# Kernel tuning notes

Measured on AMD Instinct MI355X. Metric: run time of the kernel, lower is better.

The kernel has to match this reference:

```python
import jax, jax.numpy as jnp
import numpy as np
import math


def _forward(x, f0, theta, sigma, theta0, fbs, mix, w1, b1, w2, b2, conv_w):
    B, I, H, W = x.shape          # config requires B == I == H (== W here)
    S, O, _ = f0.shape            # config requires O == 1
    # ---- log-Gabor filter bank, fully vectorized over (scale, out, in) ----
    yy = jnp.linspace(-1.0, 1.0, H)[:, None]   # meshgrid 'ij': y along rows
    xx = jnp.linspace(-1.0, 1.0, W)[None, :]
    r = jnp.sqrt(xx ** 2 + yy ** 2 + 1e-6)     # [H,W]
    phi = jnp.arctan2(yy, xx)                  # [H,W]
    lr = jnp.log(r)
    log_gabor = jnp.exp(-(lr - jnp.log(f0)[..., None, None]) ** 2
                        / (2.0 * jnp.log(sigma)[..., None, None] ** 2))
    angular = jnp.exp(-(phi - theta[..., None, None]) ** 2
                      / (2.0 * theta0[..., None, None] ** 2))
    filters = log_gabor * angular              # [S,O,I,H,W]
    # ---- FFT (torch fftshift default shifts ALL dims; jnp matches) ----
    xs = jnp.fft.fftshift(jnp.fft.fft2(x))     # [B,I,H,W] complex64
    # ---- frequency attention (two 1x1 convs + softmax over scales) ----
    h1 = jax.nn.relu(jnp.einsum('bchw,oc->bohw', jnp.abs(xs), w1)
                     + b1[None, :, None, None])
    aw = jax.nn.softmax(jnp.einsum('bchw,sc->bshw', h1, w2)
                        + b2[None, :, None, None], axis=1)   # [B,S,H,W]
    # ---- attention-weighted combine. Faithful to torch broadcasting with
    # O==1 and B==I: attended[0,b,i,h,w] = sum_s xs[b,i]*F[s,0,i]*aw[i,s] ----
    attended = jnp.einsum('bihw,sihw,ishw->bihw', xs, filters[:, 0], aw)[None]
    # ---- dynamic frequency band mask (torch slices dims 2,3 = (Cin,H)) ----
    s_idx = jnp.floor((fbs[0, :, 0] + 1.0) / 2.0 * H).astype(jnp.int32)  # [I]
    e_idx = jnp.floor((fbs[0, :, 1] + 1.0) / 2.0 * H).astype(jnp.int32)
    arI = jnp.arange(I)
    arH = jnp.arange(H)
    mk = (arI[None, :] >= s_idx[:, None]) & (arI[None, :] < e_idx[:, None])  # [J,I]
    mh = (arH[None, :] >= s_idx[:, None]) & (arH[None, :] < e_idx[:, None])  # [J,H]
    mask = (mk[:, :, None] & mh[:, None, :]).astype(x.dtype)                 # [J,I,H]
    attended = attended * mask[None, :, :, :, None]
    # ---- back to spatial domain ----
    x_filtered = jnp.fft.ifft2(jnp.fft.ifftshift(attended)).real  # [1,B,I,H,W]
    # ---- spatial 3x3 conv path ----
    x_spatial = jax.lax.conv_general_dilated(
        x, conv_w, window_strides=(1, 1), padding=((1, 1), (1, 1)),
        dimension_numbers=('NCHW', 'OIHW', 'NCHW'))               # [B,1,H,W]
    return mix * x_filtered + (1.0 - mix) * x_spatial[None]


def setup_inputs() -> dict:
    key = jax.random.key(0)
    ks = jax.random.split(key, 10)
    B = I = H = W = 64
    O, S, HID = 1, 3, 64
    PI = math.pi
    x = jax.random.normal(ks[0], (B, I, H, W), dtype=jnp.float32)
    f0 = jnp.ones((S, O, I), jnp.float32)
    theta0 = jnp.ones((S, O, I), jnp.float32)
    sigma = jax.random.uniform(ks[1], (S, O, I), jnp.float32) * PI
    theta = jax.random.uniform(ks[2], (S, O, I), jnp.float32) * PI
    fbs = jax.random.uniform(ks[3], (O, I, 2), jnp.float32)
    mix = jax.random.uniform(ks[4], (1,), jnp.float32)
    w1 = jax.random.normal(ks[5], (HID, I), jnp.float32) * 0.05
    b1 = jnp.zeros((HID,), jnp.float32)
    w2 = jax.random.normal(ks[6], (S, HID), jnp.float32) * 0.05
    b2 = jnp.zeros((S,), jnp.float32)
    conv_w = jax.random.normal(ks[7], (O, I, 3, 3), jnp.float32) / math.sqrt(I * 9)
    return {'x': x, 'f0': f0, 'theta': theta, 'sigma': sigma, 'theta0': theta0,
            'fbs': fbs, 'mix': mix, 'w1': w1, 'b1': b1, 'w2': w2, 'b2': b2,
            'conv_w': conv_w}


def reference(x, f0, theta, sigma, theta0, fbs, mix, w1, b1, w2, b2, conv_w):
    return _forward(x, f0, theta, sigma, theta0, fbs, mix, w1, b1, w2, b2, conv_w)
```

## Files before the change

### kernel.cpp

```cpp
#include <hip/hip_runtime.h>

#define PI_D 3.14159265358979323846

namespace {
constexpr float CT[33] = {
  1.0000000000f,  0.9951847267f,  0.9807852804f,  0.9569403357f,
  0.9238795325f,  0.8819212643f,  0.8314696123f,  0.7730104534f,
  0.7071067812f,  0.6343932842f,  0.5555702330f,  0.4713967368f,
  0.3826834324f,  0.2902846773f,  0.1950903220f,  0.0980171403f,
  0.0f,          -0.0980171403f, -0.1950903220f, -0.2902846773f,
 -0.3826834324f, -0.4713967368f, -0.5555702330f, -0.6343932842f,
 -0.7071067812f, -0.7730104534f, -0.8314696123f, -0.8819212643f,
 -0.9238795325f, -0.9569403357f, -0.9807852804f, -0.9951847267f,
 -1.0f};
constexpr float STb[33] = {
  0.0f,           0.0980171403f,  0.1950903220f,  0.2902846773f,
  0.3826834324f,  0.4713967368f,  0.5555702330f,  0.6343932842f,
  0.7071067812f,  0.7730104534f,  0.8314696123f,  0.8819212643f,
  0.9238795325f,  0.9569403357f,  0.9807852804f,  0.9951847267f,
  1.0f,           0.9951847267f,  0.9807852804f,  0.9569403357f,
  0.9238795325f,  0.8819212643f,  0.8314696123f,  0.7730104534f,
  0.7071067812f,  0.6343932842f,  0.5555702330f,  0.4713967368f,
  0.3826834324f,  0.2902846773f,  0.1950903220f,  0.0980171403f,
  0.0f};
}

__device__ __forceinline__ void bitrev64(float v[64]) {
#pragma unroll
  for (int i = 0; i < 64; ++i) {
    const int j = (int)(__brev((unsigned)i) >> 26);
    if (j > i) { const float tv = v[i]; v[i] = v[j]; v[j] = tv; }
  }
}

template <bool INV, bool REAL>
__device__ __forceinline__ void fft64_stages(float re[64], float im[64]) {
#pragma unroll
  for (int s = 0; s < 6; ++s) {
    const int half = 1 << s;
    const int m = half << 1;
    const int tstep = 32 >> s;
#pragma unroll
    for (int k = 0; k < 64; k += m) {
#pragma unroll
      for (int j = 0; j < half; ++j) {
        const int ti = j * tstep;
        const int a = k + j, b = k + j + half;
        if (REAL && j == 0) {
          const float tr = re[b];
          re[b] = re[a] - tr;
          re[a] = re[a] + tr;
        } else if (REAL && ti == 16) {
          const float t0 = re[b];
          re[b] = re[a];
          im[b] = t0;
          im[a] = -t0;
        } else {
          float tr, tii;
          if (ti == 0) {
            tr = re[b]; tii = im[b];
          } else if (ti == 16) {
            if (INV) { tr = -im[b]; tii = re[b]; }
            else     { tr =  im[b]; tii = -re[b]; }
          } else {
            const float wr = CT[ti];
            const float wi = INV ? STb[ti] : -STb[ti];
            tr  = re[b] * wr - im[b] * wi;
            tii = re[b] * wi + im[b] * wr;
          }
          re[b] = re[a] - tr;  im[b] = im[a] - tii;
          re[a] = re[a] + tr;  im[a] = im[a] + tii;
        }
      }
    }
  }
}

template <bool INV>
__device__ __forceinline__ void fft64_regs(float re[64], float im[64]) {
  bitrev64(re);
  bitrev64(im);
  fft64_stages<INV, false>(re, im);
}

__device__ __forceinline__ void fft64_fwd_real(float re[64], float im[64]) {
  bitrev64(re);
  fft64_stages<false, true>(re, im);
}

__device__ __forceinline__ void band_from_fbs(const float* __restrict__ fbs,
                                              int c, int& s0, int& e0) {
  s0 = (int)floorf((fbs[2 * c]     + 1.0f) * 0.5f * 64.0f);
  e0 = (int)floorf((fbs[2 * c + 1] + 1.0f) * 0.5f * 64.0f);
}

__global__ __launch_bounds__(64) void k_fft_fwd(const float* __restrict__ x,
                                                float* __restrict__ F,
                                                const float* __restrict__ fbs,
                                                const float* __restrict__ w1,
                                                float* __restrict__ w1T) {
  __shared__ float buf[64][65];
  const int t = threadIdx.x;
  const int img = blockIdx.x;
  if (img == 0) {
    for (int k = 0; k < 64; ++k) w1T[t * 64 + k] = w1[k * 64 + t];
  }
  const float* xp = x + ((size_t)img << 12);
  const float4* xr4 = reinterpret_cast<const float4*>(xp + (t << 6));
  float re[64], im[64];
#pragma unroll
  for (int q = 0; q < 16; ++q) {
    const float4 v = xr4[q];
    re[4 * q]     = v.x; re[4 * q + 1] = v.y;
    re[4 * q + 2] = v.z; re[4 * q + 3] = v.w;
  }
#pragma unroll
  for (int j = 0; j < 64; ++j) im[j] = 0.0f;
  fft64_fwd_real(re, im);
#pragma unroll
  for (int j = 0; j < 64; ++j) buf[t][j] = re[j];
  __syncthreads();
#pragma unroll
  for (int j = 0; j < 64; ++j) re[j] = buf[j][t];
  __syncthreads();
#pragma unroll
  for (int j = 0; j < 64; ++j) buf[t][j] = im[j];
  __syncthreads();
#pragma unroll
  for (int j = 0; j < 64; ++j) im[j] = buf[j][t];
  fft64_regs<false>(re, im);
  const int b = img >> 6, i = img & 63;
  const int b_s = (b + 32) & 63, i_s = (i + 32) & 63;
  int s0, e0;
  band_from_fbs(fbs, b_s, s0, e0);
  float* Fre = F + ((size_t)img << 13);
  if ((i_s >= s0) && (i_s < e0)) {
    float* Fim = Fre + 4096;
#pragma unroll
    for (int j = 0; j < 64; ++j) {
      Fre[j * 64 + t] = re[j];
      Fim[j * 64 + t] = im[j];
    }
  } else {
#pragma unroll
    for (int j = 0; j < 64; ++j)
      Fre[j * 64 + t] = sqrtf(re[j] * re[j] + im[j] * im[j]);
  }
}

__global__ __launch_bounds__(128) void k_attn_conv(
    const float* __restrict__ F, const float* __restrict__ w1T,
    const float* __restrict__ b1, const float* __restrict__ w2,
    const float* __restrict__ b2, const float* __restrict__ f0,
    const float* __restrict__ theta, const float* __restrict__ sigma,
    const float* __restrict__ theta0, const float* __restrict__ fbs,
    float* __restrict__ Wc,
    const float* __restrict__ x, const float* __restrict__ cw,
    const float* __restrict__ mixp, float* __restrict__ xsp,
    float* __restrict__ out) {
  __shared__ float4 part4[64][17];
  const int t = threadIdx.x;
  const unsigned blk = blockIdx.x;
  const unsigned q3 = blk / 3u;
  const unsigned r3 = blk - q3 * 3u;

  if (r3 == 2u) {
    float* wsm = reinterpret_cast<float*>(part4);
    for (int q = t; q < 576; q += 128) wsm[q] = cw[q];
    __syncthreads();
    const int lane = t & 63;
    const int wv = t >> 6;
    const int b = (int)(q3 >> 5);
    const int row = (int)((q3 & 31u) << 1) | wv;
    const float* xb = x + ((size_t)b << 18);
    const int rm = row > 0 ? row - 1 : 0;
    const int rp = row < 63 ? row + 1 : 63;
    float P00 = 0.f, P01 = 0.f, P02 = 0.f;
    float P10 = 0.f, P11 = 0.f, P12 = 0.f;
    float P20 = 0.f, P21 = 0.f, P22 = 0.f;
#pragma unroll 4
    for (int ch = 0; ch < 64; ++ch) {
      const float* xc = xb + (ch << 12);
      const float v0 = xc[(rm << 6) + lane];
      const float v1 = xc[(row << 6) + lane];
      const float v2 = xc[(rp << 6) + lane];
      const float* wp = &wsm[ch * 9];
      P00 = fmaf(v0, wp[0], P00);
      P01 = fmaf(v0, wp[1], P01);
      P02 = fmaf(v0, wp[2], P02);
      P10 = fmaf(v1, wp[3], P10);
      P11 = fmaf(v1, wp[4], P11);
      P12 = fmaf(v1, wp[5], P12);
      P20 = fmaf(v2, wp[6], P20);
      P21 = fmaf(v2, wp[7], P21);
      P22 = fmaf(v2, wp[8], P22);
    }
    const float tmask = (row > 0) ? 1.0f : 0.0f;
    const float bmask = (row < 63) ? 1.0f : 0.0f;
    const float Ql = tmask * P00 + P10 + bmask * P20;
    const float Qm = tmask * P01 + P11 + bmask * P21;
    const float Qr = tmask * P02 + P12 + bmask * P22;
    const float fromL = __shfl_up(Ql, 1, 64);
    const float fromR = __shfl_down(Qr, 1, 64);
    float acc = Qm;
    if (lane > 0) acc += fromL;
    if (lane < 63) acc += fromR;
    xsp[((size_t)b << 12) + (row << 6) + lane] = acc;
    const int b_s = (b + 32) & 63;
    int s0, e0;
    band_from_fbs(fbs, b_s, s0, e0);
    const float val = (1.0f - mixp[0]) * acc;
    float* ob = out + ((size_t)b << 18) + (row << 6) + lane;
#pragma unroll 4
    for (int i2 = 0; i2 < 64; ++i2) {
      const int i_s = (i2 + 32) & 63;
      if (!(i_s >= s0 && i_s < e0)) ob[(size_t)i2 << 12] = val;
    }
    return;
  }

  const int ai = (int)(2u * q3 + r3);
  const int lane = t & 63;
  const int wv = __builtin_amdgcn_readfirstlane(t >> 6);
  const int i = ai >> 6;
  const int h = ai & 63;
  const int b_f = (i + 32) & 63;
  const int u_f = (h + 32) & 63;
  const int v_f = (lane + 32) & 63;
  const int pos_f = (u_f << 6) + v_f;
  int s0a, e0a;
  band_from_fbs(fbs, i, s0a, e0a);
  const int c0 = wv << 5, c1 = c0 + 32;
  int alo = s0a < c0 ? c0 : (s0a > c1 ? c1 : s0a);
  int ahi = e0a < c0 ? c0 : (e0a > c1 ? c1 : e0a);
  if (ahi < alo) ahi = alo;
  float acc[64];
#pragma unroll
  for (int k = 0; k < 64; ++k) acc[k] = 0.0f;
  const float* Fb = F + ((size_t)(b_f << 6) << 13) + pos_f;
#pragma unroll 4
  for (int c = c0; c < alo; ++c) {
    const int c_f = (c + 32) & 63;
    const float mc = Fb[(size_t)c_f << 13];
    const float* wrow = w1T + (c << 6);
#pragma unroll
    for (int k = 0; k < 64; ++k) acc[k] = fmaf(wrow[k], mc, acc[k]);
  }
#pragma unroll 2
  for (int c = alo; c < ahi; ++c) {
    const int c_f = (c + 32) & 63;
    const float* base = Fb + ((size_t)c_f << 13);
    const float xr = base[0], xi = base[4096];
    const float mc = sqrtf(xr * xr + xi * xi);
    const float* wrow = w1T + (c << 6);
#pragma unroll
    for (int k = 0; k < 64; ++k) acc[k] = fmaf(wrow[k], mc, acc[k]);
  }
#pragma unroll 4
  for (int c = ahi; c < c1; ++c) {
    const int c_f = (c + 32) & 63;
    const float mc = Fb[(size_t)c_f << 13];
    const float* wrow = w1T + (c << 6);
#pragma unroll
    for (int k = 0; k < 64; ++k) acc[k] = fmaf(wrow[k], mc, acc[k]);
  }
  if (wv != 0) {
#pragma unroll
    for (int kk = 0; kk < 16; ++kk)
      part4[lane][kk] = make_float4(acc[4 * kk], acc[4 * kk + 1],
                                    acc[4 * kk + 2], acc[4 * kk + 3]);
  }
  __syncthreads();
  if (wv != 0) return;
#pragma unroll
  for (int kk = 0; kk < 16; ++kk) {
    const float4 p = part4[lane][kk];
    acc[4 * kk] += p.x; acc[4 * kk + 1] += p.y;
    acc[4 * kk + 2] += p.z; acc[4 * kk + 3] += p.w;
  }
  float l0 = b2[0], l1 = b2[1], l2 = b2[2];
#pragma unroll
  for (int k = 0; k < 64; ++k) {
    const float hv = fmaxf(acc[k] + b1[k], 0.0f);
    l0 = fmaf(w2[k], hv, l0);
    l1 = fmaf(w2[64 + k], hv, l1);
    l2 = fmaf(w2[128 + k], hv, l2);
  }
  float mx = fmaxf(l0, fmaxf(l1, l2));
  float e0v = expf(l0 - mx), e1 = expf(l1 - mx), e2 = expf(l2 - mx);
  float inv = 1.0f / (e0v + e1 + e2);
  float aw0 = e0v * inv, aw1 = e1 * inv, aw2 = e2 * inv;
  const float yy = -1.0f + (float)h * (2.0f / 63.0f);
  const float xx = -1.0f + (float)lane * (2.0f / 63.0f);
  const float r = sqrtf(xx * xx + yy * yy + 1e-6f);
  const float lr = logf(r);
  const float phi = atan2f(yy, xx);
  float wc = 0.0f;
  const float aws[3] = {aw0, aw1, aw2};
#pragma unroll
  for (int s = 0; s < 3; ++s) {
    const float f0v = f0[s * 64 + i];
    const float sgv = sigma[s * 64 + i];
    const float thv = theta[s * 64 + i];
    const float t0v = theta0[s * 64 + i];
    const float ls = logf(sgv);
    const float d1 = lr - logf(f0v);
    const float g1 = expf(-(d1 * d1) / (2.0f * ls * ls));
    const float d2 = phi - thv;
    const float g2 = expf(-(d2 * d2) / (2.0f * t0v * t0v));
    wc = fmaf(g1 * g2, aws[s], wc);
  }
  Wc[((i << 6) + h) * 64 + lane] = wc;
}

__global__ __launch_bounds__(64) void k_ifft_act(
    const float* __restrict__ F, const float* __restrict__ Wc,
    const float* __restrict__ xsp, const float* __restrict__ fbs,
    const float* __restrict__ mixp, float* __restrict__ out) {
  const int img = blockIdx.x;
  const int b = img >> 6, i = img & 63;
  const int b_s = (b + 32) & 63, i_s = (i + 32) & 63;
  int s0, e0;
  band_from_fbs(fbs, b_s, s0, e0);
  if (!((i_s >= s0) && (i_s < e0))) return;
  __shared__ float buf[64][65];
  const int t = threadIdx.x;
  const float* Fre = F + ((size_t)img << 13);
  const float* Fim = Fre + 4096;
  const float* Wcp = Wc + ((size_t)i_s << 12);
  const int u_s = (t + 32) & 63;
  const float rmask = (u_s >= s0 && u_s < e0) ? 1.0f : 0.0f;
  const float* wrow = Wcp + (u_s << 6);
  const float4* fr4 = reinterpret_cast<const float4*>(Fre + (t << 6));
  const float4* fi4 = reinterpret_cast<const float4*>(Fim + (t << 6));
  float re[64], im[64];
#pragma unroll
  for (int q = 0; q < 16; ++q) {
    const int j0 = 4 * q;
    const float4 w4 = *reinterpret_cast<const float4*>(wrow + ((j0 + 32) & 63));
    const float4 vr = fr4[q];
    const float4 vi = fi4[q];
    const float w0 = rmask * w4.x, w1v = rmask * w4.y;
    const float w2v = rmask * w4.z, w3v = rmask * w4.w;
    re[j0]     = vr.x * w0;  re[j0 + 1] = vr.y * w1v;
    re[j0 + 2] = vr.z * w2v; re[j0 + 3] = vr.w * w3v;
    im[j0]     = vi.x * w0;  im[j0 + 1] = vi.y * w1v;
    im[j0 + 2] = vi.z * w2v; im[j0 + 3] = vi.w * w3v;
  }
  fft64_regs<true>(re, im);
#pragma unroll
  for (int j = 0; j < 64; ++j) buf[t][j] = re[j];
  __syncthreads();
#pragma unroll
  for (int j = 0; j < 64; ++j) re[j] = buf[j][t];
  __syncthreads();
#pragma unroll
  for (int j = 0; j < 64; ++j) buf[t][j] = im[j];
  __syncthreads();
#pragma unroll
  for (int j = 0; j < 64; ++j) im[j] = buf[j][t];
  fft64_regs<true>(re, im);
  const float mixv = mixp[0];
  const float sc = mixv * (1.0f / 4096.0f);
  const float om = 1.0f - mixv;
  float* op = out + ((size_t)img << 12);
  const float* xp = xsp + ((size_t)b << 12);
#pragma unroll
  for (int j = 0; j < 64; ++j)
    op[j * 64 + t] = fmaf(sc, re[j], om * xp[j * 64 + t]);
}

extern "C" void kernel_launch(void* const* d_in, const int* in_sizes, int n_in,
                              void* d_out, int out_size, void* d_ws, size_t ws_size,
                              hipStream_t stream) {
  const float* x      = (const float*)d_in[0];
  const float* f0     = (const float*)d_in[1];
  const float* theta  = (const float*)d_in[2];
  const float* sigma  = (const float*)d_in[3];
  const float* theta0 = (const float*)d_in[4];
  const float* fbs    = (const float*)d_in[5];
  const float* mix    = (const float*)d_in[6];
  const float* w1     = (const float*)d_in[7];
  const float* b1     = (const float*)d_in[8];
  const float* w2     = (const float*)d_in[9];
  const float* b2     = (const float*)d_in[10];
  const float* cw     = (const float*)d_in[11];
  float* out = (float*)d_out;
  char* ws = (char*)d_ws;
  float* F   = (float*)(ws);
  float* Wc  = (float*)(ws + 134217728);
  float* xsp = (float*)(ws + 134217728 + 1048576);
  float* w1T = (float*)(ws + 134217728 + 2097152);

  k_fft_fwd<<<4096, 64, 0, stream>>>(x, F, fbs, w1, w1T);
  k_attn_conv<<<6144, 128, 0, stream>>>(F, w1T, b1, w2, b2, f0, theta, sigma,
                                        theta0, fbs, Wc, x, cw, mix, xsp, out);
  k_ifft_act<<<4096, 64, 0, stream>>>(F, Wc, xsp, fbs, mix, out);
}
```

Before: 214.6 us.

## Use single-wave blocks for attention and conv, dropping split-K LDS reduction

The fused attention/conv kernel now runs with 64-thread blocks. Each attention wave accumulates all 64 input channels itself, so the two-wave channel split, the LDS partial-sum exchange and the barrier are gone. Conv blocks now handle one row per wave and read conv weights straight from global memory instead of staging them in LDS. Blocks alternate between attention and conv work. The change removes LDS traffic and synchronisation, but doubles the serial channel loop per wave and halves the parallelism per attention output.

```diff
diff --git a/kernel.cpp b/kernel.cpp
--- a/kernel.cpp
+++ b/kernel.cpp
@@ -148,7 +148,7 @@
   }
 }
 
-__global__ __launch_bounds__(128) void k_attn_conv(
+__global__ __launch_bounds__(64, 4) void k_attn_conv(
     const float* __restrict__ F, const float* __restrict__ w1T,
     const float* __restrict__ b1, const float* __restrict__ w2,
     const float* __restrict__ b2, const float* __restrict__ f0,
@@ -158,20 +158,14 @@
     const float* __restrict__ x, const float* __restrict__ cw,
     const float* __restrict__ mixp, float* __restrict__ xsp,
     float* __restrict__ out) {
-  __shared__ float4 part4[64][17];
   const int t = threadIdx.x;
   const unsigned blk = blockIdx.x;
-  const unsigned q3 = blk / 3u;
-  const unsigned r3 = blk - q3 * 3u;
-
-  if (r3 == 2u) {
-    float* wsm = reinterpret_cast<float*>(part4);
-    for (int q = t; q < 576; q += 128) wsm[q] = cw[q];
-    __syncthreads();
-    const int lane = t & 63;
-    const int wv = t >> 6;
-    const int b = (int)(q3 >> 5);
-    const int row = (int)((q3 & 31u) << 1) | wv;
+  const unsigned id = blk >> 1;
+
+  if (blk & 1u) {
+    const int lane = t;
+    const int b = (int)(id >> 6);
+    const int row = (int)(id & 63u);
     const float* xb = x + ((size_t)b << 18);
     const int rm = row > 0 ? row - 1 : 0;
     const int rp = row < 63 ? row + 1 : 63;
@@ -184,7 +178,7 @@
       const float v0 = xc[(rm << 6) + lane];
       const float v1 = xc[(row << 6) + lane];
       const float v2 = xc[(rp << 6) + lane];
-      const float* wp = &wsm[ch * 9];
+      const float* wp = cw + ch * 9;
       P00 = fmaf(v0, wp[0], P00);
       P01 = fmaf(v0, wp[1], P01);
       P02 = fmaf(v0, wp[2], P02);
@@ -219,9 +213,8 @@
     return;
   }
 
-  const int ai = (int)(2u * q3 + r3);
-  const int lane = t & 63;
-  const int wv = __builtin_amdgcn_readfirstlane(t >> 6);
+  const int ai = (int)id;
+  const int lane = t;
   const int i = ai >> 6;
   const int h = ai & 63;
   const int b_f = (i + 32) & 63;
@@ -230,16 +223,15 @@
   const int pos_f = (u_f << 6) + v_f;
   int s0a, e0a;
   band_from_fbs(fbs, i, s0a, e0a);
-  const int c0 = wv << 5, c1 = c0 + 32;
-  int alo = s0a < c0 ? c0 : (s0a > c1 ? c1 : s0a);
-  int ahi = e0a < c0 ? c0 : (e0a > c1 ? c1 : e0a);
+  int alo = s0a < 0 ? 0 : (s0a > 64 ? 64 : s0a);
+  int ahi = e0a < 0 ? 0 : (e0a > 64 ? 64 : e0a);
   if (ahi < alo) ahi = alo;
   float acc[64];
 #pragma unroll
   for (int k = 0; k < 64; ++k) acc[k] = 0.0f;
   const float* Fb = F + ((size_t)(b_f << 6) << 13) + pos_f;
 #pragma unroll 4
-  for (int c = c0; c < alo; ++c) {
+  for (int c = 0; c < alo; ++c) {
     const int c_f = (c + 32) & 63;
     const float mc = Fb[(size_t)c_f << 13];
     const float* wrow = w1T + (c << 6);
@@ -257,26 +249,12 @@
     for (int k = 0; k < 64; ++k) acc[k] = fmaf(wrow[k], mc, acc[k]);
   }
 #pragma unroll 4
-  for (int c = ahi; c < c1; ++c) {
+  for (int c = ahi; c < 64; ++c) {
     const int c_f = (c + 32) & 63;
     const float mc = Fb[(size_t)c_f << 13];
     const float* wrow = w1T + (c << 6);
 #pragma unroll
     for (int k = 0; k < 64; ++k) acc[k] = fmaf(wrow[k], mc, acc[k]);
-  }
-  if (wv != 0) {
-#pragma unroll
-    for (int kk = 0; kk < 16; ++kk)
-      part4[lane][kk] = make_float4(acc[4 * kk], acc[4 * kk + 1],
-                                    acc[4 * kk + 2], acc[4 * kk + 3]);
-  }
-  __syncthreads();
-  if (wv != 0) return;
-#pragma unroll
-  for (int kk = 0; kk < 16; ++kk) {
-    const float4 p = part4[lane][kk];
-    acc[4 * kk] += p.x; acc[4 * kk + 1] += p.y;
-    acc[4 * kk + 2] += p.z; acc[4 * kk + 3] += p.w;
   }
   float l0 = b2[0], l1 = b2[1], l2 = b2[2];
 #pragma unroll
@@ -393,7 +371,7 @@
   float* w1T = (float*)(ws + 134217728 + 2097152);
 
   k_fft_fwd<<<4096, 64, 0, stream>>>(x, F, fbs, w1, w1T);
-  k_attn_conv<<<6144, 128, 0, stream>>>(F, w1T, b1, w2, b2, f0, theta, sigma,
-                                        theta0, fbs, Wc, x, cw, mix, xsp, out);
+  k_attn_conv<<<8192, 64, 0, stream>>>(F, w1T, b1, w2, b2, f0, theta, sigma,
+                                       theta0, fbs, Wc, x, cw, mix, xsp, out);
   k_ifft_act<<<4096, 64, 0, stream>>>(F, Wc, xsp, fbs, mix, out);
 }
```

Measured after the change: 234.0 us. +9.1%, slower.
